# Optimization experiments

Measured on AMD Instinct MI355X. Metric: run time of the kernel, lower is better.

The kernel has to match this reference:

```python
import jax, jax.numpy as jnp
import numpy as np
import functools

N, D, R, E, L, C, MAXDEG = 40000, 128, 3, 640000, 2, 40, 512
BN_EPS = 1e-5


def setup_inputs():
    ks = iter(jax.random.split(jax.random.key(0), 40))
    nrm = lambda s, sc=0.05: jax.random.normal(next(ks), s, dtype=jnp.float32) * sc
    x = jax.random.normal(next(ks), (N, D), dtype=jnp.float32)
    edge_indices = jax.random.randint(next(ks), (R, 2, E), 0, N, dtype=jnp.int32)
    out_emb = nrm((L, MAXDEG, D)).at[:, 0].set(0.0)  # padding_idx=0 -> zero row
    in_emb = nrm((L, MAXDEG, D)).at[:, 0].set(0.0)
    return dict(
        x=x, edge_indices=edge_indices,
        W_src=nrm((L, D, D)), b_src=nrm((L, D)),
        W_dst=nrm((L, D, D)), b_dst=nrm((L, D)),
        W_outf=nrm((L, D)), b_outf=nrm((L,)),
        W_inf=nrm((L, D)), b_inf=nrm((L,)),
        W_fc=nrm((L, D, D)), b_fc=nrm((L, D)),
        bn_gamma=jnp.ones((L, D), jnp.float32), bn_beta=jnp.zeros((L, D), jnp.float32),
        out_deg_emb=out_emb, in_deg_emb=in_emb,
        out_mask=jnp.ones((R, N), jnp.float32), out_mask_bias=jnp.zeros((R, N), jnp.float32),
        in_mask=jnp.ones((R, N), jnp.float32), in_mask_bias=jnp.zeros((R, N), jnp.float32),
        alpha=jnp.float32(0.5), tau=jnp.float32(0.0),
        W_lin=nrm((D, C)), b_lin=nrm((C,)),
    )


def _forward(x, W_src, b_src, W_dst, b_dst, W_outf, b_outf, W_inf, b_inf,
             W_fc, b_fc, bn_gamma, bn_beta, out_deg_emb, in_deg_emb,
             out_mask, out_mask_bias, in_mask, in_mask_bias, alpha, tau,
             W_lin, b_lin, edge_indices):
    seg = lambda d, i: jax.ops.segment_sum(d, i, num_segments=N)
    # source builds I with arange(0, N-1): identity with last diagonal entry missing
    i_mask = (jnp.arange(N) < N - 1).astype(jnp.float32)[:, None]

    rel = []
    for r in range(R):
        row, col = edge_indices[r, 0], edge_indices[r, 1]
        ones = jnp.ones(E, jnp.float32)
        out_deg, in_deg = seg(ones, row), seg(ones, col)
        ods = jnp.where(out_deg > 0, 1.0 / jnp.sqrt(jnp.maximum(out_deg, 1.0)), 0.0)
        ids_ = jnp.where(in_deg > 0, 1.0 / jnp.sqrt(jnp.maximum(in_deg, 1.0)), 0.0)
        # 'dir' norm: D_out^{-1/2} A D_in^{-1/2}; the transposed adj shares the same edge weights
        w = ods[row] * ids_[col]
        rel.append((row, col, w,
                    jnp.clip(out_deg, 0, MAXDEG - 1).astype(jnp.int32),
                    jnp.clip(in_deg, 0, MAXDEG - 1).astype(jnp.int32)))

    def spmm(r_, y):  # adj_norm @ y : gather cols, scatter-add to rows
        row, col, w = rel[r_][0], rel[r_][1], rel[r_][2]
        return seg(w[:, None] * y[col], row)

    def spmm_t(r_, y):  # adj_norm^T @ y
        row, col, w = rel[r_][0], rel[r_][1], rel[r_][2]
        return seg(w[:, None] * y[row], col)

    def dirichlet(mm, y):
        x1 = y / (jnp.sum(jnp.abs(y), axis=1, keepdims=True) + 1e-12)  # row_l1_normalize
        x1sq = x1 * x1
        return (i_mask * x1sq + mm(x1sq)) - 2.0 * ((i_mask * x1 + mm(x1)) * x1 - x1sq)

    eff_tau = jnp.exp(tau) + 0.1

    def conv(l, h):
        out = jnp.zeros((N, D), h.dtype)
        cis, cos_ = [], []
        for r in range(R):
            mm = functools.partial(spmm, r)
            mmt = functools.partial(spmm_t, r)
            out_nei, in_nei = mm(h), mmt(h)
            e_out, e_in = dirichlet(mm, h), dirichlet(mmt, h)
            c_out = (-e_out + out_deg_emb[l][rel[r][3]]) @ W_outf[l] + b_outf[l]  # [N]
            c_in = (-e_in + in_deg_emb[l][rel[r][4]]) @ W_inf[l] + b_inf[l]
            cm = jax.nn.softmax(jnp.stack([c_out, c_in], axis=1) / eff_tau, axis=1)  # tau_softmax
            c_out = cm[:, 0] * out_mask[r] + out_mask_bias[r]
            c_in = cm[:, 1] * in_mask[r] + in_mask_bias[r]
            out = out + c_out[:, None] * (out_nei @ W_src[l] + b_src[l]) \
                      + c_in[:, None] * (in_nei @ W_dst[l] + b_dst[l])
            cis.append(c_in)
            cos_.append(c_out)
        out = out / R
        # F.pad(x,(0,dim-x.shape[1])) is a no-op since input_dim == output_dim
        output = out + alpha * (h @ W_fc[l] + b_fc[l])
        mu, var = jnp.mean(output, axis=0), jnp.var(output, axis=0)  # BatchNorm1d (train mode)
        output = (output - mu) / jnp.sqrt(var + BN_EPS) * bn_gamma[l] + bn_beta[l]
        return output, jnp.mean(jnp.stack(cis), 0)[:, None], jnp.mean(jnp.stack(cos_), 0)[:, None]

    pos_h, neg_h = x, x
    pos_hs, neg_hs, gs, cins, couts = [], [], [], [], []
    for l in range(L):
        ph, ci, co = conv(l, pos_h)
        ph = jax.nn.relu(ph)  # jumping_knowledge truthy -> relu every layer; dropout p=0
        perm = jax.random.permutation(jax.random.key(100 + l), N)  # torch.randperm
        nh, _, _ = conv(l, neg_h[perm])
        nh = jax.nn.relu(nh)
        pos_h, neg_h = ph, nh
        pos_hs.append(ph)
        neg_hs.append(nh)
        gs.append(jnp.mean(ph, axis=0, keepdims=True))
        cins.append(ci)
        couts.append(co)
    c_ins = jnp.mean(jnp.stack(cins), 0)
    c_outs = jnp.mean(jnp.stack(couts), 0)
    jk = functools.reduce(jnp.maximum, pos_hs)  # JumpingKnowledge mode='max'
    logp = jax.nn.log_softmax(jk @ W_lin + b_lin, axis=1)
    return (logp, c_ins, c_outs, *pos_hs, *neg_hs, *gs)


def reference(x, edge_indices, W_src, b_src, W_dst, b_dst, W_outf, b_outf,
              W_inf, b_inf, W_fc, b_fc, bn_gamma, bn_beta, out_deg_emb,
              in_deg_emb, out_mask, out_mask_bias, in_mask, in_mask_bias,
              alpha, tau, W_lin, b_lin):
    return _forward(x, W_src, b_src, W_dst, b_dst, W_outf, b_outf, W_inf, b_inf,
                    W_fc, b_fc, bn_gamma, bn_beta, out_deg_emb, in_deg_emb,
                    out_mask, out_mask_bias, in_mask, in_mask_bias, alpha, tau,
                    W_lin, b_lin, edge_indices)
```

## Files before the change

### kernel.cpp

```cpp
#include <hip/hip_runtime.h>

constexpr int Nn = 40000;
constexpr int Dd = 128;
constexpr int Rr = 3;
constexpr int Ee = 640000;
constexpr int Ll = 2;
constexpr int Cc = 40;
constexpr int MAXD = 512;
constexpr float BN_EPS = 1e-5f;

constexpr int RB_ELEMS = 1024;
constexpr int RB_NB = (Nn + RB_ELEMS - 1) / RB_ELEMS;
constexpr int RB_BINS = 256;

constexpr int EB_ELEMS = 4096;
constexpr int EB_NB = (Ee + EB_ELEMS - 1) / EB_ELEMS;
constexpr int EB_H = 256 * EB_NB;

constexpr int HR_BINS = 13334;
constexpr int HR_PAD = 13344;
constexpr int HR_SB = 16;
constexpr int HR_CHUNK = (Ee + HR_SB - 1) / HR_SB;

__device__ __forceinline__ unsigned rotl32(unsigned x, int d) { return (x << d) | (x >> (32 - d)); }

__device__ void threefry2x32(unsigned k0, unsigned k1, unsigned c0, unsigned c1,
                             unsigned& o0, unsigned& o1) {
  unsigned ks2 = k0 ^ k1 ^ 0x1BD11BDAu;
  unsigned x0 = c0 + k0, x1 = c1 + k1;
#define TFR4(a,b,c,d2) \
  x0 += x1; x1 = rotl32(x1,a);  x1 ^= x0; \
  x0 += x1; x1 = rotl32(x1,b);  x1 ^= x0; \
  x0 += x1; x1 = rotl32(x1,c);  x1 ^= x0; \
  x0 += x1; x1 = rotl32(x1,d2); x1 ^= x0;
  TFR4(13,15,26,6);  x0 += k1;  x1 += ks2 + 1u;
  TFR4(17,29,16,24); x0 += ks2; x1 += k0 + 2u;
  TFR4(13,15,26,6);  x0 += k0;  x1 += k1 + 3u;
  TFR4(17,29,16,24); x0 += k1;  x1 += ks2 + 4u;
  TFR4(13,15,26,6);  x0 += ks2; x1 += k0 + 5u;
#undef TFR4
  o0 = x0; o1 = x1;
}

__global__ void k_genkeys(unsigned* __restrict__ keys, unsigned seed, int rounds,
                          int* __restrict__ vout, int doIota) {
  int i = blockIdx.x * blockDim.x + threadIdx.x;
  if (i >= Nn) return;
  unsigned k0 = 0u, k1 = seed, sk0 = 0u, sk1 = 0u;
  for (int rd = 0; rd < rounds; rd++) {
    unsigned a0, a1, b0, b1;
    threefry2x32(k0, k1, 0u, 0u, a0, a1);
    threefry2x32(k0, k1, 0u, 1u, b0, b1);
    sk0 = b0; sk1 = b1;
    k0 = a0; k1 = a1;
  }
  unsigned o0, o1;
  threefry2x32(sk0, sk1, 0u, (unsigned)i, o0, o1);
  keys[i] = o0 ^ o1;
  if (doIota) vout[i] = i;
}

__global__ void k_rhist(const unsigned* __restrict__ keys, int* __restrict__ hist, int shift) {
  __shared__ int lh[RB_BINS];
  int t = threadIdx.x;
  lh[t] = 0;
  __syncthreads();
  int base = blockIdx.x * RB_ELEMS;
  for (int i = t; i < RB_ELEMS; i += 256) {
    int g = base + i;
    if (g < Nn) atomicAdd(&lh[(keys[g] >> shift) & 255], 1);
  }
  __syncthreads();
  hist[t * RB_NB + blockIdx.x] = lh[t];
}

__device__ void scan_body(const int* cnt, int* off, int n, int items) {
  int t = threadIdx.x;
  int lo = t * items, hi = min(lo + items, n);
  int s = 0;
  for (int i = lo; i < hi; i++) s += cnt[i];
  int lane = t & 63, wid = t >> 6;
  int sc = s;
#pragma unroll
  for (int o = 1; o < 64; o <<= 1) {
    int v = __shfl_up(sc, o);
    if (lane >= o) sc += v;
  }
  __shared__ int wsum[16], woff[16];
  if (lane == 63) wsum[wid] = sc;
  __syncthreads();
  if (t == 0) {
    int a = 0;
    for (int w = 0; w < 16; w++) { woff[w] = a; a += wsum[w]; }
    off[n] = a;
  }
  __syncthreads();
  int run = woff[wid] + sc - s;
  for (int i = lo; i < hi; i++) {
    int v = cnt[i];
    off[i] = run;
    run += v;
  }
}

__global__ __launch_bounds__(1024) void k_scanN(const int* __restrict__ cnt, int* __restrict__ off,
                                                int n, int items) {
  scan_body(cnt, off, n, items);
}

__global__ __launch_bounds__(1024) void k_scan6(const int* __restrict__ odeg, const int* __restrict__ ideg,
                                                int* __restrict__ csr_off, int* __restrict__ csc_off) {
  int b = blockIdx.x;
  const int* cnt = (b < 3) ? (odeg + b * Nn) : (ideg + (b - 3) * Nn);
  int* off = (b < 3) ? (csr_off + b * (Nn + 1)) : (csc_off + (b - 3) * (Nn + 1));
  scan_body(cnt, off, Nn, (Nn + 1023) / 1024);
}

__global__ void k_rscatter(const unsigned* __restrict__ keys, const int* __restrict__ vals,
                           const int* __restrict__ scanned, int shift,
                           unsigned* __restrict__ okeys, int* __restrict__ ovals) {
  __shared__ int running[RB_BINS];
  __shared__ int wcount[4][RB_BINS];
  __shared__ int dbase[RB_BINS];
  int t = threadIdx.x;
  int lane = t & 63, w = t >> 6;
  running[t] = 0;
  dbase[t] = scanned[t * RB_NB + blockIdx.x];
  int base = blockIdx.x * RB_ELEMS;
  for (int rnd = 0; rnd < 4; rnd++) {
#pragma unroll
    for (int q = 0; q < 4; q++) wcount[q][t] = 0;
    __syncthreads();
    int g = base + rnd * 256 + t;
    bool valid = g < Nn;
    unsigned key = valid ? keys[g] : 0u;
    int d = (key >> shift) & 255;
    unsigned long long bb = __ballot(valid);
    unsigned long long mask = bb;
#pragma unroll
    for (int k = 0; k < 8; k++) {
      bool b = (d >> k) & 1;
      unsigned long long tt = __ballot(b && valid);
      mask &= b ? tt : ~tt;
    }
    mask &= bb;
    int riw = __popcll(mask & ((1ull << lane) - 1ull));
    int cnt_ = __popcll(mask);
    if (valid && riw == 0) wcount[w][d] = cnt_;
    __syncthreads();
    if (valid) {
      int prior = 0;
#pragma unroll
      for (int ww = 0; ww < 4; ww++) if (ww < w) prior += wcount[ww][d];
      int gp = dbase[d] + running[d] + prior + riw;
      okeys[gp] = key;
      ovals[gp] = vals[g];
    }
    __syncthreads();
    running[t] += wcount[0][t] + wcount[1][t] + wcount[2][t] + wcount[3][t];
    __syncthreads();
  }
}

__global__ void k_permrows(const float* __restrict__ src, const int* __restrict__ perm,
                           float* __restrict__ dst) {
  int row = blockIdx.x * 8 + (threadIdx.x >> 5);
  int lane = threadIdx.x & 31;
  if (row >= Nn) return;
  int p = perm[row];
  ((float4*)(dst + (size_t)row * Dd))[lane] = ((const float4*)(src + (size_t)p * Dd))[lane];
}

__global__ __launch_bounds__(256) void k_hist2(const int* __restrict__ ei, int* __restrict__ partials) {
  __shared__ int lh[HR_BINS];
  int bid = blockIdx.x;
  int sb = bid % HR_SB;
  int range = (bid / HR_SB) % 3;
  int j = bid / (3 * HR_SB);
  int rel = j >> 1, which = j & 1;
  const int* src = ei + (size_t)rel * 2 * Ee + (size_t)which * Ee;
  int lo = range * HR_BINS;
  for (int i = threadIdx.x; i < HR_BINS; i += 256) lh[i] = 0;
  __syncthreads();
  int e0 = sb * HR_CHUNK, e1 = min(e0 + HR_CHUNK, Ee);
  for (int e = e0 + threadIdx.x; e < e1; e += 256) {
    int v = src[e] - lo;
    if (v >= 0 && v < HR_BINS) atomicAdd(&lh[v], 1);
  }
  __syncthreads();
  int* dst = partials + (size_t)bid * HR_PAD;
  for (int i = threadIdx.x; i < HR_BINS; i += 256) dst[i] = lh[i];
}

__global__ void k_hreduce(const int* __restrict__ partials, int* __restrict__ odeg,
                          int* __restrict__ ideg) {
  int idx = blockIdx.x * 256 + threadIdx.x;
  if (idx >= 6 * Nn) return;
  int j = idx / Nn, bin = idx - j * Nn;
  int range = bin / HR_BINS, off = bin - range * HR_BINS;
  const int* p = partials + (size_t)((j * 3 + range) * HR_SB) * HR_PAD + off;
  int sum = 0;
#pragma unroll
  for (int b = 0; b < HR_SB; b++) sum += p[(size_t)b * HR_PAD];
  int rel = j >> 1;
  (j & 1 ? ideg : odeg)[rel * Nn + bin] = sum;
}

__global__ void k_degnorm(const int* __restrict__ odeg, const int* __restrict__ ideg,
                          float* __restrict__ ods, float* __restrict__ ids,
                          int* __restrict__ odix, int* __restrict__ idix) {
  int idx = blockIdx.x * blockDim.x + threadIdx.x;
  if (idx >= Rr * Nn) return;
  int od = odeg[idx], id_ = ideg[idx];
  ods[idx] = od > 0 ? 1.0f / sqrtf((float)od) : 0.0f;
  ids[idx] = id_ > 0 ? 1.0f / sqrtf((float)id_) : 0.0f;
  odix[idx] = od < MAXD - 1 ? od : MAXD - 1;
  idix[idx] = id_ < MAXD - 1 ? id_ : MAXD - 1;
}

__global__ void k_pack(const int* __restrict__ ei, unsigned* __restrict__ pcsr,
                       unsigned* __restrict__ pcsc) {
  int idx = blockIdx.x * 256 + threadIdx.x;
  if (idx >= 3 * Ee) return;
  int r = idx / Ee, e = idx - r * Ee;
  const int* base = ei + (size_t)r * 2 * Ee;
  unsigned rw = (unsigned)base[e], cl = (unsigned)base[Ee + e];
  pcsr[idx] = (rw << 16) | cl;
  pcsc[idx] = (cl << 16) | rw;
}

__global__ __launch_bounds__(256) void k_ehist(const unsigned* __restrict__ pin,
                                               int* __restrict__ hist, int shift) {
  __shared__ int lh[256];
  int a = blockIdx.x / EB_NB, blk = blockIdx.x % EB_NB;
  const unsigned* src = pin + (size_t)a * Ee;
  lh[threadIdx.x] = 0;
  __syncthreads();
  int base = blk * EB_ELEMS;
  for (int i = threadIdx.x; i < EB_ELEMS; i += 256) {
    int g = base + i;
    if (g < Ee) atomicAdd(&lh[(src[g] >> shift) & 255], 1);
  }
  __syncthreads();
  hist[(size_t)a * EB_H + threadIdx.x * EB_NB + blk] = lh[threadIdx.x];
}

__global__ __launch_bounds__(1024) void k_escan6(const int* __restrict__ hist, int* __restrict__ esc) {
  int a = blockIdx.x;
  scan_body(hist + (size_t)a * EB_H, esc + (size_t)a * (EB_H + 1), EB_H, (EB_H + 1023) / 1024);
}

__global__ __launch_bounds__(256) void k_escatter(const unsigned* __restrict__ pin,
                                                  const int* __restrict__ esc, int shift,
                                                  unsigned* __restrict__ pout) {
  __shared__ int running[256];
  __shared__ int wcount[4][256];
  __shared__ int dbase[256];
  int a = blockIdx.x / EB_NB, blk = blockIdx.x % EB_NB;
  const unsigned* src = pin + (size_t)a * Ee;
  unsigned* dst = pout + (size_t)a * Ee;
  int t = threadIdx.x;
  int lane = t & 63, w = t >> 6;
  running[t] = 0;
  dbase[t] = esc[(size_t)a * (EB_H + 1) + t * EB_NB + blk];
  int base = blk * EB_ELEMS;
  for (int rnd = 0; rnd < 16; rnd++) {
#pragma unroll
    for (int q = 0; q < 4; q++) wcount[q][t] = 0;
    __syncthreads();
    int g = base + rnd * 256 + t;
    bool valid = g < Ee;
    unsigned key = valid ? src[g] : 0u;
    int d = (key >> shift) & 255;
    unsigned long long bb = __ballot(valid);
    unsigned long long mask = bb;
#pragma unroll
    for (int k = 0; k < 8; k++) {
      bool b = (d >> k) & 1;
      unsigned long long tt = __ballot(b && valid);
      mask &= b ? tt : ~tt;
    }
    mask &= bb;
    int riw = __popcll(mask & ((1ull << lane) - 1ull));
    int cnt_ = __popcll(mask);
    if (valid && riw == 0) wcount[w][d] = cnt_;
    __syncthreads();
    if (valid) {
      int prior = 0;
#pragma unroll
      for (int ww = 0; ww < 4; ww++) if (ww < w) prior += wcount[ww][d];
      int gp = dbase[d] + running[d] + prior + riw;
      dst[gp] = key;
    }
    __syncthreads();
    running[t] += wcount[0][t] + wcount[1][t] + wcount[2][t] + wcount[3][t];
    __syncthreads();
  }
}

__global__ void k_rowscalar(const float* __restrict__ h, const float* __restrict__ Wfo,
                            const float* __restrict__ Wfi, float4* __restrict__ aux) {
  int wid = (blockIdx.x * blockDim.x + threadIdx.x) >> 6;
  int lane = threadIdx.x & 63;
  if (wid >= Nn) return;
  float2 a = ((const float2*)(h + (size_t)wid * Dd))[lane];
  float2 wo = ((const float2*)Wfo)[lane];
  float2 wi = ((const float2*)Wfi)[lane];
  float l1 = fabsf(a.x) + fabsf(a.y);
  float so = a.x * a.x * wo.x + a.y * a.y * wo.y;
  float si = a.x * a.x * wi.x + a.y * a.y * wi.y;
#pragma unroll
  for (int o = 32; o; o >>= 1) {
    l1 += __shfl_xor(l1, o);
    so += __shfl_xor(so, o);
    si += __shfl_xor(si, o);
  }
  if (lane == 0) {
    float ri = 1.0f / (l1 + 1e-12f);
    aux[wid] = make_float4(ri, ri * ri * so, ri * ri * si, 0.f);
  }
}

__global__ void k_lut(const float* __restrict__ eo, const float* __restrict__ ei_,
                      const float* __restrict__ Wfo, const float* __restrict__ Wfi,
                      float* __restrict__ luto, float* __restrict__ luti) {
  int wid = (blockIdx.x * blockDim.x + threadIdx.x) >> 6;
  int lane = threadIdx.x & 63;
  if (wid >= MAXD) return;
  float2 a = ((const float2*)(eo + (size_t)wid * Dd))[lane];
  float2 b = ((const float2*)(ei_ + (size_t)wid * Dd))[lane];
  float2 wo = ((const float2*)Wfo)[lane];
  float2 wi = ((const float2*)Wfi)[lane];
  float so = a.x * wo.x + a.y * wo.y;
  float si = b.x * wi.x + b.y * wi.y;
#pragma unroll
  for (int o = 32; o; o >>= 1) { so += __shfl_xor(so, o); si += __shfl_xor(si, o); }
  if (lane == 0) { luto[wid] = so; luti[wid] = si; }
}

__global__ __launch_bounds__(512) void k_csrdir3(
    const int* __restrict__ csr_off, const unsigned* __restrict__ pcsr,
    const int* __restrict__ csc_off, const unsigned* __restrict__ pcsc,
    const float* __restrict__ ods_r, const float* __restrict__ ids_r,
    const float4* __restrict__ aux, const float* __restrict__ h,
    const float* __restrict__ Wfo, const float* __restrict__ Wfi,
    const float* __restrict__ luto, const float* __restrict__ luti,
    const int* __restrict__ odix, const int* __restrict__ idix,
    const float* __restrict__ bo, const float* __restrict__ bi,
    const float* __restrict__ taup,
    const float* __restrict__ omask, const float* __restrict__ omaskb,
    const float* __restrict__ imask, const float* __restrict__ imaskb,
    float* __restrict__ Tout, float* __restrict__ Tin,
    float* __restrict__ sco, float* __restrict__ sci,
    float* __restrict__ co_acc, float* __restrict__ ci_acc,
    int first, int is_pos) {
  __shared__ float lq[8], lp[8], lc[8];
  int t = threadIdx.x;
  int wv = t >> 6, lane = t & 63;
  int dir = wv >> 2;
  int n = blockIdx.x * 4 + (wv & 3);
  const int* off = dir ? csc_off : csr_off;
  const unsigned* nbrp = dir ? pcsc : pcsr;
  const float* scn = dir ? ods_r : ids_r;
  float a_self = (dir ? ids_r : ods_r)[n];
  const float* Wf = dir ? Wfi : Wfo;
  int s0 = off[n], s1 = off[n + 1];
  int hl = lane & 31, half = lane >> 5;
  float4 wf4 = ((const float4*)Wf)[hl];
  float4 hn4 = ((const float4*)(h + (size_t)n * Dd))[hl];
  float rn = aux[n].x;
  float4 s = make_float4(0.f, 0.f, 0.f, 0.f);
  float4 pa = make_float4(0.f, 0.f, 0.f, 0.f);
  float qacc = 0.f;
  for (int base = s0; base < s1; base += 64) {
    int eidx = base + lane;
    bool valid = eidx < s1;
    int mi = valid ? (int)(pcsr[0], nbrp[eidx] & 0xFFFFu) : 0;
    float4 av = valid ? aux[mi] : make_float4(0.f, 0.f, 0.f, 0.f);
    float scv = valid ? scn[mi] : 0.f;
    float qsel = dir ? av.z : av.y;
    int cnt = min(64, s1 - base);
    for (int j = half; j < cnt; j += 2) {
      int m = __shfl(mi, j);
      float sc = __shfl(scv, j);
      float rm = __shfl(av.x, j);
      float qv = __shfl(qsel, j);
      float w = a_self * sc;
      float wrm = w * rm;
      float4 hv = ((const float4*)(h + (size_t)m * Dd))[hl];
      s.x += w * hv.x; s.y += w * hv.y; s.z += w * hv.z; s.w += w * hv.w;
      pa.x += wrm * hv.x; pa.y += wrm * hv.y; pa.z += wrm * hv.z; pa.w += wrm * hv.w;
      qacc += w * qv;
    }
  }
  s.x += __shfl_xor(s.x, 32); s.y += __shfl_xor(s.y, 32);
  s.z += __shfl_xor(s.z, 32); s.w += __shfl_xor(s.w, 32);
  pa.x += __shfl_xor(pa.x, 32); pa.y += __shfl_xor(pa.y, 32);
  pa.z += __shfl_xor(pa.z, 32); pa.w += __shfl_xor(pa.w, 32);
  qacc += __shfl_xor(qacc, 32);
  float pd = rn * (hn4.x * wf4.x * pa.x + hn4.y * wf4.y * pa.y +
                   hn4.z * wf4.z * pa.z + hn4.w * wf4.w * pa.w);
#pragma unroll
  for (int o = 16; o; o >>= 1) pd += __shfl_xor(pd, o);
  if (lane == 0) { lq[wv] = qacc; lp[wv] = pd; }
  __syncthreads();
  if (t < 4) {
    int nn = blockIdx.x * 4 + t;
    float Qo_ = lq[t], Po_ = lp[t], Qi_ = lq[4 + t], Pi_ = lp[4 + t];
    float4 a2 = aux[nn];
    float im = (nn < Nn - 1) ? 1.0f : 0.0f;
    float so_ = luto[odix[nn]] + bo[0] - (Qo_ - 2.0f * Po_ + (2.0f - im) * a2.y);
    float si_ = luti[idix[nn]] + bi[0] - (Qi_ - 2.0f * Pi_ + (2.0f - im) * a2.z);
    float tt = expf(taup[0]) + 0.1f;
    float aa = so_ / tt, bb = si_ / tt;
    float mm = fmaxf(aa, bb);
    float ea = expf(aa - mm), eb = expf(bb - mm);
    float inv = 1.0f / (ea + eb);
    float co = ea * inv * omask[nn] + omaskb[nn];
    float ci = eb * inv * imask[nn] + imaskb[nn];
    lc[t] = co; lc[4 + t] = ci;
    if (first) { sco[nn] = co; sci[nn] = ci; }
    else       { sco[nn] += co; sci[nn] += ci; }
    if (is_pos) { co_acc[nn] += co; ci_acc[nn] += ci; }
  }
  __syncthreads();
  float c = lc[wv];
  if (lane < 32) {
    float* T = dir ? Tin : Tout;
    size_t o = (size_t)n * Dd;
    float4 v = make_float4(c * s.x, c * s.y, c * s.z, c * s.w);
    if (!first) {
      float4 old = ((const float4*)(T + o))[hl];
      v.x += old.x; v.y += old.y; v.z += old.z; v.w += old.w;
    }
    ((float4*)(T + o))[hl] = v;
  }
}

__global__ __launch_bounds__(256) void k_gemmconv(
    const float* __restrict__ Tout, const float* __restrict__ Tin, const float* __restrict__ h,
    const float* __restrict__ Wsrc, const float* __restrict__ Wdst, const float* __restrict__ Wfc,
    const float* __restrict__ bsrc, const float* __restrict__ bdst, const float* __restrict__ bfc,
    const float* __restrict__ sco, const float* __restrict__ sci,
    const float* __restrict__ alphap, float* __restrict__ pre) {
  __shared__ float Asm[64][36];
  __shared__ float Bsm[32][132];
  int t = threadIdx.x;
  int rg = t >> 5, cg = t & 31;
  int m0 = blockIdx.x * 64;
  int arow = t >> 2, aq = t & 3;
  float alpha = alphap[0];
  float acc[8][4];
#pragma unroll
  for (int r = 0; r < 8; r++)
#pragma unroll
    for (int c = 0; c < 4; c++) acc[r][c] = 0.f;
  for (int kt = 0; kt < 12; kt++) {
    int sec = kt >> 2, kc = (kt & 3) * 32;
    const float* Ap = sec == 0 ? Tout : (sec == 1 ? Tin : h);
    const float* Wp = sec == 0 ? Wsrc : (sec == 1 ? Wdst : Wfc);
    float sA = (sec == 2) ? alpha : (1.0f / (float)Rr);
    __syncthreads();
    {
      const float4* src = (const float4*)(Ap + (size_t)(m0 + arow) * Dd + kc + aq * 8);
      float4 v0 = src[0], v1 = src[1];
      float4* d0 = (float4*)&Asm[arow][aq * 8];
      d0[0] = make_float4(v0.x * sA, v0.y * sA, v0.z * sA, v0.w * sA);
      d0[1] = make_float4(v1.x * sA, v1.y * sA, v1.z * sA, v1.w * sA);
    }
#pragma unroll
    for (int j = 0; j < 4; j++) {
      int idx = t + j * 256;
      int k = idx >> 5, d4 = idx & 31;
      *(float4*)&Bsm[k][d4 * 4] = *(const float4*)(Wp + (size_t)(kc + k) * Dd + d4 * 4);
    }
    __syncthreads();
#pragma unroll
    for (int kk = 0; kk < 32; kk += 4) {
      float4 af[8], bf[4];
#pragma unroll
      for (int r = 0; r < 8; r++) af[r] = *(const float4*)&Asm[rg * 8 + r][kk];
#pragma unroll
      for (int j = 0; j < 4; j++) bf[j] = *(const float4*)&Bsm[kk + j][cg * 4];
#pragma unroll
      for (int r = 0; r < 8; r++) {
        const float* ap = (const float*)&af[r];
#pragma unroll
        for (int j = 0; j < 4; j++) {
          const float* bp = (const float*)&bf[j];
          acc[r][0] += ap[j] * bp[0];
          acc[r][1] += ap[j] * bp[1];
          acc[r][2] += ap[j] * bp[2];
          acc[r][3] += ap[j] * bp[3];
        }
      }
    }
  }
  float4 vb1 = *(const float4*)(bsrc + cg * 4);
  float4 vb2 = *(const float4*)(bdst + cg * 4);
  float4 vbf = *(const float4*)(bfc + cg * 4);
#pragma unroll
  for (int r = 0; r < 8; r++) {
    int row = m0 + rg * 8 + r;
    size_t o = (size_t)row * Dd + cg * 4;
    float s1 = sco[row] * (1.0f / (float)Rr), s2 = sci[row] * (1.0f / (float)Rr);
    float4 v;
    v.x = acc[r][0] + s1 * vb1.x + s2 * vb2.x + alpha * vbf.x;
    v.y = acc[r][1] + s1 * vb1.y + s2 * vb2.y + alpha * vbf.y;
    v.z = acc[r][2] + s1 * vb1.z + s2 * vb2.z + alpha * vbf.z;
    v.w = acc[r][3] + s1 * vb1.w + s2 * vb2.w + alpha * vbf.w;
    *(float4*)(pre + o) = v;
  }
}

__global__ void k_bnstats(const float* __restrict__ pre, float* __restrict__ sums) {
  __shared__ float ls[256], ls2[256];
  int c = threadIdx.x & 127, sub = threadIdx.x >> 7;
  float s = 0.f, s2 = 0.f;
  for (int n = blockIdx.x * 2 + sub; n < Nn; n += gridDim.x * 2) {
    float v = pre[(size_t)n * Dd + c];
    s += v; s2 += v * v;
  }
  ls[threadIdx.x] = s; ls2[threadIdx.x] = s2;
  __syncthreads();
  if (sub == 0) {
    atomicAdd(&sums[c], ls[c] + ls[c + 128]);
    atomicAdd(&sums[c + 128], ls2[c] + ls2[c + 128]);
  }
}

__global__ void k_bnapply(const float* __restrict__ pre, const float* __restrict__ sums,
                          const float* __restrict__ gamma, const float* __restrict__ beta,
                          float* __restrict__ hout, float* __restrict__ gs, int do_gs) {
  __shared__ float ls[256];
  int c = threadIdx.x & 127, sub = threadIdx.x >> 7;
  float mu = sums[c] * (1.0f / (float)Nn);
  float var = sums[c + 128] * (1.0f / (float)Nn) - mu * mu;
  float sc = gamma[c] / sqrtf(var + BN_EPS);
  float bt = beta[c];
  float g = 0.f;
  for (int n = blockIdx.x * 2 + sub; n < Nn; n += gridDim.x * 2) {
    float v = (pre[(size_t)n * Dd + c] - mu) * sc + bt;
    v = fmaxf(v, 0.f);
    hout[(size_t)n * Dd + c] = v;
    g += v;
  }
  if (do_gs) {
    ls[threadIdx.x] = g;
    __syncthreads();
    if (sub == 0) atomicAdd(&gs[c], (ls[c] + ls[c + 128]) * (1.0f / (float)Nn));
  }
}

__global__ void k_cio(const float* __restrict__ ci_acc, const float* __restrict__ co_acc,
                      float* __restrict__ cins, float* __restrict__ couts) {
  int n = blockIdx.x * blockDim.x + threadIdx.x;
  if (n < Nn) {
    cins[n] = ci_acc[n] * (1.0f / (float)(Ll * Rr));
    couts[n] = co_acc[n] * (1.0f / (float)(Ll * Rr));
  }
}

__global__ __launch_bounds__(64) void k_logp(const float* __restrict__ ph0, const float* __restrict__ ph1,
                      const float* __restrict__ Wlin, const float* __restrict__ blin,
                      float* __restrict__ logp) {
  __shared__ float jk[Dd];
  __shared__ float lg[Cc];
  int n = blockIdx.x, t = threadIdx.x;
  for (int d = t; d < Dd; d += 64) jk[d] = fmaxf(ph0[(size_t)n * Dd + d], ph1[(size_t)n * Dd + d]);
  __syncthreads();
  if (t < Cc) {
    float acc = blin[t];
    for (int k = 0; k < Dd; k++) acc += jk[k] * Wlin[k * Cc + t];
    lg[t] = acc;
  }
  __syncthreads();
  float m = -1e30f;
  for (int c = 0; c < Cc; c++) m = fmaxf(m, lg[c]);
  float s = 0.f;
  for (int c = 0; c < Cc; c++) s += expf(lg[c] - m);
  float lse = m + logf(s);
  if (t < Cc) logp[(size_t)n * Cc + t] = lg[t] - lse;
}

extern "C" void kernel_launch(void* const* d_in, const int* in_sizes, int n_in,
                              void* d_out, int out_size, void* d_ws, size_t ws_size,
                              hipStream_t stream) {
  const float* x      = (const float*)d_in[0];
  const int*   ei     = (const int*)d_in[1];
  const float* W_src  = (const float*)d_in[2];
  const float* b_src  = (const float*)d_in[3];
  const float* W_dst  = (const float*)d_in[4];
  const float* b_dst  = (const float*)d_in[5];
  const float* W_outf = (const float*)d_in[6];
  const float* b_outf = (const float*)d_in[7];
  const float* W_inf  = (const float*)d_in[8];
  const float* b_inf  = (const float*)d_in[9];
  const float* W_fc   = (const float*)d_in[10];
  const float* b_fc   = (const float*)d_in[11];
  const float* gamma  = (const float*)d_in[12];
  const float* beta   = (const float*)d_in[13];
  const float* oemb   = (const float*)d_in[14];
  const float* iemb   = (const float*)d_in[15];
  const float* omask  = (const float*)d_in[16];
  const float* omaskb = (const float*)d_in[17];
  const float* imask  = (const float*)d_in[18];
  const float* imaskb = (const float*)d_in[19];
  const float* alphap = (const float*)d_in[20];
  const float* taup   = (const float*)d_in[21];
  const float* Wlin   = (const float*)d_in[22];
  const float* blin   = (const float*)d_in[23];

  float* out   = (float*)d_out;
  float* logp  = out;
  float* cins  = logp + (size_t)Nn * Cc;
  float* couts = cins + Nn;
  float* ph0   = couts + Nn;
  float* ph1   = ph0 + (size_t)Nn * Dd;
  float* nh0   = ph1 + (size_t)Nn * Dd;
  float* nh1   = nh0 + (size_t)Nn * Dd;
  float* gs0   = nh1 + (size_t)Nn * Dd;
  float* gs1   = gs0 + Dd;

  char* p = (char*)d_ws;
  auto alloc = [&](size_t bytes) -> void* {
    void* q = (void*)p;
    p += (bytes + 255) & ~(size_t)255;
    return q;
  };
  float* pre   = (float*)alloc((size_t)Nn * Dd * 4);
  float* Tout  = (float*)alloc((size_t)Nn * Dd * 4);
  float* Tin   = (float*)alloc((size_t)Nn * Dd * 4);
  float* hperm = (float*)alloc((size_t)Nn * Dd * 4);
  unsigned* pbuf = (unsigned*)alloc((size_t)6 * Ee * 4);
  size_t qwords = (size_t)6 * Ee;
  size_t pwords = (size_t)(6 * 3 * HR_SB) * HR_PAD;
  unsigned* qbuf = (unsigned*)alloc((qwords > pwords ? qwords : pwords) * 4);
  int* partials = (int*)qbuf;
  int* csr_off = (int*)alloc((size_t)Rr * (Nn + 1) * 4);
  int* csc_off = (int*)alloc((size_t)Rr * (Nn + 1) * 4);
  int* odeg    = (int*)alloc((size_t)Rr * Nn * 4);
  int* ideg    = (int*)alloc((size_t)Rr * Nn * 4);
  float* ods   = (float*)alloc((size_t)Rr * Nn * 4);
  float* ids   = (float*)alloc((size_t)Rr * Nn * 4);
  int* odix    = (int*)alloc((size_t)Rr * Nn * 4);
  int* idix    = (int*)alloc((size_t)Rr * Nn * 4);
  float4* aux  = (float4*)alloc((size_t)Nn * 16);
  float* sco   = (float*)alloc((size_t)Nn * 4 * 2);
  float* sci   = sco + Nn;
  float* coacc = (float*)alloc((size_t)Nn * 4 * 2);
  float* ciacc = coacc + Nn;
  float* luto  = (float*)alloc(MAXD * 4);
  float* luti  = (float*)alloc(MAXD * 4);
  float* bnsum = (float*)alloc(256 * 4);
  unsigned* kbuf0 = (unsigned*)alloc((size_t)Nn * 4);
  unsigned* kbuf1 = (unsigned*)alloc((size_t)Nn * 4);
  int* vbuf0 = (int*)alloc((size_t)Nn * 4);
  int* vbuf1 = (int*)alloc((size_t)Nn * 4);
  int* rhist = (int*)alloc((size_t)(RB_BINS * RB_NB + 1) * 4);
  int* rscan = (int*)alloc((size_t)(RB_BINS * RB_NB + 1) * 4);
  int* ehist = (int*)alloc((size_t)6 * EB_H * 4);
  int* escan = (int*)alloc((size_t)6 * (EB_H + 1) * 4);

  k_hist2<<<6 * 3 * HR_SB, 256, 0, stream>>>(ei, partials);
  k_hreduce<<<(6 * Nn + 255) / 256, 256, 0, stream>>>(partials, odeg, ideg);
  k_degnorm<<<(Rr * Nn + 255) / 256, 256, 0, stream>>>(odeg, ideg, ods, ids, odix, idix);
  k_scan6<<<6, 1024, 0, stream>>>(odeg, ideg, csr_off, csc_off);
  k_pack<<<(3 * Ee + 255) / 256, 256, 0, stream>>>(ei, pbuf, pbuf + (size_t)3 * Ee);
  k_ehist<<<6 * EB_NB, 256, 0, stream>>>(pbuf, ehist, 16);
  k_escan6<<<6, 1024, 0, stream>>>(ehist, escan);
  k_escatter<<<6 * EB_NB, 256, 0, stream>>>(pbuf, escan, 16, qbuf);
  k_ehist<<<6 * EB_NB, 256, 0, stream>>>(qbuf, ehist, 24);
  k_escan6<<<6, 1024, 0, stream>>>(ehist, escan);
  k_escatter<<<6 * EB_NB, 256, 0, stream>>>(qbuf, escan, 24, pbuf);
  hipMemsetAsync(coacc, 0, (size_t)Nn * 4 * 2, stream);

  auto radix4 = [&]() {
    for (int pass = 0; pass < 4; pass++) {
      const unsigned* ik = (pass & 1) ? kbuf1 : kbuf0;
      const int*      iv = (pass & 1) ? vbuf1 : vbuf0;
      unsigned*       ok = (pass & 1) ? kbuf0 : kbuf1;
      int*            ov = (pass & 1) ? vbuf0 : vbuf1;
      int shift = pass * 8;
      k_rhist<<<RB_NB, 256, 0, stream>>>(ik, rhist, shift);
      k_scanN<<<1, 1024, 0, stream>>>(rhist, rscan, RB_BINS * RB_NB, (RB_BINS * RB_NB + 1023) / 1024);
      k_rscatter<<<RB_NB, 256, 0, stream>>>(ik, iv, rscan, shift, ok, ov);
    }
  };

  auto make_perm = [&](unsigned seed) {
    k_genkeys<<<(Nn + 255) / 256, 256, 0, stream>>>(kbuf0, seed, 1, vbuf0, 1);
    radix4();
    k_genkeys<<<(Nn + 255) / 256, 256, 0, stream>>>(kbuf0, seed, 2, vbuf0, 0);
    radix4();
  };

  auto conv = [&](int l, const float* hin, float* hout, float* gs, int is_pos) {
    const float* Wfo = W_outf + l * Dd;
    const float* Wfi = W_inf + l * Dd;
    k_rowscalar<<<Nn / 4, 256, 0, stream>>>(hin, Wfo, Wfi, aux);
    for (int r = 0; r < Rr; r++) {
      k_csrdir3<<<Nn / 4, 512, 0, stream>>>(csr_off + r * (Nn + 1), pbuf + (size_t)r * Ee,
                                            csc_off + r * (Nn + 1), pbuf + (size_t)(3 + r) * Ee,
                                            ods + r * Nn, ids + r * Nn, aux, hin, Wfo, Wfi,
                                            luto, luti, odix + r * Nn, idix + r * Nn,
                                            b_outf + l, b_inf + l, taup,
                                            omask + (size_t)r * Nn, omaskb + (size_t)r * Nn,
                                            imask + (size_t)r * Nn, imaskb + (size_t)r * Nn,
                                            Tout, Tin, sco, sci, coacc, ciacc,
                                            r == 0 ? 1 : 0, is_pos);
    }
    k_gemmconv<<<Nn / 64, 256, 0, stream>>>(Tout, Tin, hin,
                                            W_src + (size_t)l * Dd * Dd, W_dst + (size_t)l * Dd * Dd,
                                            W_fc + (size_t)l * Dd * Dd,
                                            b_src + l * Dd, b_dst + l * Dd, b_fc + l * Dd,
                                            sco, sci, alphap, pre);
    hipMemsetAsync(bnsum, 0, 256 * 4, stream);
    k_bnstats<<<256, 256, 0, stream>>>(pre, bnsum);
    if (is_pos) hipMemsetAsync(gs, 0, Dd * 4, stream);
    k_bnapply<<<256, 256, 0, stream>>>(pre, bnsum, gamma + l * Dd, beta + l * Dd, hout, gs, is_pos);
  };

  k_lut<<<MAXD / 4, 256, 0, stream>>>(oemb, iemb, W_outf, W_inf, luto, luti);
  conv(0, x, ph0, gs0, 1);
  make_perm(100u);
  k_permrows<<<Nn / 8, 256, 0, stream>>>(x, vbuf0, hperm);
  conv(0, hperm, nh0, nullptr, 0);

  k_lut<<<MAXD / 4, 256, 0, stream>>>(oemb + (size_t)MAXD * Dd, iemb + (size_t)MAXD * Dd,
                                      W_outf + Dd, W_inf + Dd, luto, luti);
  conv(1, ph0, ph1, gs1, 1);
  make_perm(101u);
  k_permrows<<<Nn / 8, 256, 0, stream>>>(nh0, vbuf0, hperm);
  conv(1, hperm, nh1, nullptr, 0);

  k_cio<<<(Nn + 255) / 256, 256, 0, stream>>>(ciacc, coacc, cins, couts);
  k_logp<<<Nn, 64, 0, stream>>>(ph0, ph1, Wlin, blin, logp);
}
```

Measured before the change: 2.473 ms.

## Fuse per-relation SpMM launches into one kernel and fold BN stats into GEMM

```diff
diff --git a/kernel.cpp b/kernel.cpp
--- a/kernel.cpp
+++ b/kernel.cpp
@@ -338,102 +338,109 @@
   if (lane == 0) { luto[wid] = so; luti[wid] = si; }
 }
 
-__global__ __launch_bounds__(512) void k_csrdir3(
-    const int* __restrict__ csr_off, const unsigned* __restrict__ pcsr,
-    const int* __restrict__ csc_off, const unsigned* __restrict__ pcsc,
-    const float* __restrict__ ods_r, const float* __restrict__ ids_r,
+__global__ __launch_bounds__(512) void k_csrdir4(
+    const int* __restrict__ csr_off_all, const int* __restrict__ csc_off_all,
+    const unsigned* __restrict__ pbuf,
+    const float* __restrict__ ods_all, const float* __restrict__ ids_all,
     const float4* __restrict__ aux, const float* __restrict__ h,
     const float* __restrict__ Wfo, const float* __restrict__ Wfi,
     const float* __restrict__ luto, const float* __restrict__ luti,
-    const int* __restrict__ odix, const int* __restrict__ idix,
+    const int* __restrict__ odix_all, const int* __restrict__ idix_all,
     const float* __restrict__ bo, const float* __restrict__ bi,
     const float* __restrict__ taup,
-    const float* __restrict__ omask, const float* __restrict__ omaskb,
-    const float* __restrict__ imask, const float* __restrict__ imaskb,
+    const float* __restrict__ omask_all, const float* __restrict__ omaskb_all,
+    const float* __restrict__ imask_all, const float* __restrict__ imaskb_all,
     float* __restrict__ Tout, float* __restrict__ Tin,
     float* __restrict__ sco, float* __restrict__ sci,
-    float* __restrict__ co_acc, float* __restrict__ ci_acc,
-    int first, int is_pos) {
+    float* __restrict__ co_acc, float* __restrict__ ci_acc, int is_pos) {
   __shared__ float lq[8], lp[8], lc[8];
   int t = threadIdx.x;
   int wv = t >> 6, lane = t & 63;
   int dir = wv >> 2;
   int n = blockIdx.x * 4 + (wv & 3);
-  const int* off = dir ? csc_off : csr_off;
-  const unsigned* nbrp = dir ? pcsc : pcsr;
-  const float* scn = dir ? ods_r : ids_r;
-  float a_self = (dir ? ids_r : ods_r)[n];
+  int hl = lane & 31, half = lane >> 5;
   const float* Wf = dir ? Wfi : Wfo;
-  int s0 = off[n], s1 = off[n + 1];
-  int hl = lane & 31, half = lane >> 5;
   float4 wf4 = ((const float4*)Wf)[hl];
   float4 hn4 = ((const float4*)(h + (size_t)n * Dd))[hl];
   float rn = aux[n].x;
-  float4 s = make_float4(0.f, 0.f, 0.f, 0.f);
-  float4 pa = make_float4(0.f, 0.f, 0.f, 0.f);
-  float qacc = 0.f;
-  for (int base = s0; base < s1; base += 64) {
-    int eidx = base + lane;
-    bool valid = eidx < s1;
-    int mi = valid ? (int)(pcsr[0], nbrp[eidx] & 0xFFFFu) : 0;
-    float4 av = valid ? aux[mi] : make_float4(0.f, 0.f, 0.f, 0.f);
-    float scv = valid ? scn[mi] : 0.f;
-    float qsel = dir ? av.z : av.y;
-    int cnt = min(64, s1 - base);
-    for (int j = half; j < cnt; j += 2) {
-      int m = __shfl(mi, j);
-      float sc = __shfl(scv, j);
-      float rm = __shfl(av.x, j);
-      float qv = __shfl(qsel, j);
-      float w = a_self * sc;
-      float wrm = w * rm;
-      float4 hv = ((const float4*)(h + (size_t)m * Dd))[hl];
-      s.x += w * hv.x; s.y += w * hv.y; s.z += w * hv.z; s.w += w * hv.w;
-      pa.x += wrm * hv.x; pa.y += wrm * hv.y; pa.z += wrm * hv.z; pa.w += wrm * hv.w;
-      qacc += w * qv;
-    }
-  }
-  s.x += __shfl_xor(s.x, 32); s.y += __shfl_xor(s.y, 32);
-  s.z += __shfl_xor(s.z, 32); s.w += __shfl_xor(s.w, 32);
-  pa.x += __shfl_xor(pa.x, 32); pa.y += __shfl_xor(pa.y, 32);
-  pa.z += __shfl_xor(pa.z, 32); pa.w += __shfl_xor(pa.w, 32);
-  qacc += __shfl_xor(qacc, 32);
-  float pd = rn * (hn4.x * wf4.x * pa.x + hn4.y * wf4.y * pa.y +
-                   hn4.z * wf4.z * pa.z + hn4.w * wf4.w * pa.w);
-#pragma unroll
-  for (int o = 16; o; o >>= 1) pd += __shfl_xor(pd, o);
-  if (lane == 0) { lq[wv] = qacc; lp[wv] = pd; }
-  __syncthreads();
+  float4 Tacc = make_float4(0.f, 0.f, 0.f, 0.f);
+  float scosum = 0.f, scisum = 0.f;
+
+  for (int r = 0; r < Rr; r++) {
+    const int* off = (dir ? csc_off_all : csr_off_all) + r * (Nn + 1);
+    const unsigned* nbrp = pbuf + (size_t)(dir ? 3 + r : r) * Ee;
+    const float* ods_r = ods_all + r * Nn;
+    const float* ids_r = ids_all + r * Nn;
+    const float* scn = dir ? ods_r : ids_r;
+    float a_self = (dir ? ids_r : ods_r)[n];
+    int s0 = off[n], s1 = off[n + 1];
+    float4 s = make_float4(0.f, 0.f, 0.f, 0.f);
+    float4 pa = make_float4(0.f, 0.f, 0.f, 0.f);
+    float qacc = 0.f;
+    for (int base = s0; base < s1; base += 64) {
+      int eidx = base + lane;
+      bool valid = eidx < s1;
+      int mi = valid ? (int)(nbrp[eidx] & 0xFFFFu) : 0;
+      float4 av = valid ? aux[mi] : make_float4(0.f, 0.f, 0.f, 0.f);
+      float scv = valid ? scn[mi] : 0.f;
+      float qsel = dir ? av.z : av.y;
+      int cnt = min(64, s1 - base);
+#pragma unroll 4
+      for (int j = half; j < cnt; j += 2) {
+        int m = __shfl(mi, j);
+        float sc = __shfl(scv, j);
+        float rm = __shfl(av.x, j);
+        float qv = __shfl(qsel, j);
+        float w = a_self * sc;
+        float wrm = w * rm;
+        float4 hv = ((const float4*)(h + (size_t)m * Dd))[hl];
+        s.x += w * hv.x; s.y += w * hv.y; s.z += w * hv.z; s.w += w * hv.w;
+        pa.x += wrm * hv.x; pa.y += wrm * hv.y; pa.z += wrm * hv.z; pa.w += wrm * hv.w;
+        qacc += w * qv;
+      }
+    }
+    s.x += __shfl_xor(s.x, 32); s.y += __shfl_xor(s.y, 32);
+    s.z += __shfl_xor(s.z, 32); s.w += __shfl_xor(s.w, 32);
+    pa.x += __shfl_xor(pa.x, 32); pa.y += __shfl_xor(pa.y, 32);
+    pa.z += __shfl_xor(pa.z, 32); pa.w += __shfl_xor(pa.w, 32);
+    qacc += __shfl_xor(qacc, 32);
+    float pd = rn * (hn4.x * wf4.x * pa.x + hn4.y * wf4.y * pa.y +
+                     hn4.z * wf4.z * pa.z + hn4.w * wf4.w * pa.w);
+#pragma unroll
+    for (int o = 16; o; o >>= 1) pd += __shfl_xor(pd, o);
+    if (lane == 0) { lq[wv] = qacc; lp[wv] = pd; }
+    __syncthreads();
+    if (t < 4) {
+      int nn = blockIdx.x * 4 + t;
+      float Qo_ = lq[t], Po_ = lp[t], Qi_ = lq[4 + t], Pi_ = lp[4 + t];
+      float4 a2 = aux[nn];
+      float im = (nn < Nn - 1) ? 1.0f : 0.0f;
+      float so_ = luto[odix_all[r * Nn + nn]] + bo[0] - (Qo_ - 2.0f * Po_ + (2.0f - im) * a2.y);
+      float si_ = luti[idix_all[r * Nn + nn]] + bi[0] - (Qi_ - 2.0f * Pi_ + (2.0f - im) * a2.z);
+      float tt = expf(taup[0]) + 0.1f;
+      float aa = so_ / tt, bb = si_ / tt;
+      float mm = fmaxf(aa, bb);
+      float ea = expf(aa - mm), eb = expf(bb - mm);
+      float inv = 1.0f / (ea + eb);
+      float co = ea * inv * omask_all[r * Nn + nn] + omaskb_all[r * Nn + nn];
+      float ci = eb * inv * imask_all[r * Nn + nn] + imaskb_all[r * Nn + nn];
+      lc[t] = co; lc[4 + t] = ci;
+      scosum += co; scisum += ci;
+    }
+    __syncthreads();
+    float c = lc[wv];
+    float vx = c * s.x, vy = c * s.y, vz = c * s.z, vw = c * s.w;
+    Tacc.x += vx; Tacc.y += vy; Tacc.z += vz; Tacc.w += vw;
+  }
+
+  if (lane < 32) {
+    float* T = dir ? Tin : Tout;
+    ((float4*)(T + (size_t)n * Dd))[hl] = Tacc;
+  }
   if (t < 4) {
     int nn = blockIdx.x * 4 + t;
-    float Qo_ = lq[t], Po_ = lp[t], Qi_ = lq[4 + t], Pi_ = lp[4 + t];
-    float4 a2 = aux[nn];
-    float im = (nn < Nn - 1) ? 1.0f : 0.0f;
-    float so_ = luto[odix[nn]] + bo[0] - (Qo_ - 2.0f * Po_ + (2.0f - im) * a2.y);
-    float si_ = luti[idix[nn]] + bi[0] - (Qi_ - 2.0f * Pi_ + (2.0f - im) * a2.z);
-    float tt = expf(taup[0]) + 0.1f;
-    float aa = so_ / tt, bb = si_ / tt;
-    float mm = fmaxf(aa, bb);
-    float ea = expf(aa - mm), eb = expf(bb - mm);
-    float inv = 1.0f / (ea + eb);
-    float co = ea * inv * omask[nn] + omaskb[nn];
-    float ci = eb * inv * imask[nn] + imaskb[nn];
-    lc[t] = co; lc[4 + t] = ci;
-    if (first) { sco[nn] = co; sci[nn] = ci; }
-    else       { sco[nn] += co; sci[nn] += ci; }
-    if (is_pos) { co_acc[nn] += co; ci_acc[nn] += ci; }
-  }
-  __syncthreads();
-  float c = lc[wv];
-  if (lane < 32) {
-    float* T = dir ? Tin : Tout;
-    size_t o = (size_t)n * Dd;
-    float4 v = make_float4(c * s.x, c * s.y, c * s.z, c * s.w);
-    if (!first) {
-      float4 old = ((const float4*)(T + o))[hl];
-      v.x += old.x; v.y += old.y; v.z += old.z; v.w += old.w;
-    }
-    ((float4*)(T + o))[hl] = v;
+    sco[nn] = scosum; sci[nn] = scisum;
+    if (is_pos) { co_acc[nn] += scosum; ci_acc[nn] += scisum; }
   }
 }
 
@@ -442,9 +449,10 @@
     const float* __restrict__ Wsrc, const float* __restrict__ Wdst, const float* __restrict__ Wfc,
     const float* __restrict__ bsrc, const float* __restrict__ bdst, const float* __restrict__ bfc,
     const float* __restrict__ sco, const float* __restrict__ sci,
-    const float* __restrict__ alphap, float* __restrict__ pre) {
+    const float* __restrict__ alphap, float* __restrict__ pre, float* __restrict__ bnsum) {
   __shared__ float Asm[64][36];
   __shared__ float Bsm[32][132];
+  __shared__ float lsum[128], lsum2[128];
   int t = threadIdx.x;
   int rg = t >> 5, cg = t & 31;
   int m0 = blockIdx.x * 64;
@@ -499,6 +507,7 @@
   float4 vb1 = *(const float4*)(bsrc + cg * 4);
   float4 vb2 = *(const float4*)(bdst + cg * 4);
   float4 vbf = *(const float4*)(bfc + cg * 4);
+  float ps[4] = {0.f, 0.f, 0.f, 0.f}, ps2[4] = {0.f, 0.f, 0.f, 0.f};
 #pragma unroll
   for (int r = 0; r < 8; r++) {
     int row = m0 + rg * 8 + r;
@@ -510,23 +519,19 @@
     v.z = acc[r][2] + s1 * vb1.z + s2 * vb2.z + alpha * vbf.z;
     v.w = acc[r][3] + s1 * vb1.w + s2 * vb2.w + alpha * vbf.w;
     *(float4*)(pre + o) = v;
-  }
-}
-
-__global__ void k_bnstats(const float* __restrict__ pre, float* __restrict__ sums) {
-  __shared__ float ls[256], ls2[256];
-  int c = threadIdx.x & 127, sub = threadIdx.x >> 7;
-  float s = 0.f, s2 = 0.f;
-  for (int n = blockIdx.x * 2 + sub; n < Nn; n += gridDim.x * 2) {
-    float v = pre[(size_t)n * Dd + c];
-    s += v; s2 += v * v;
-  }
-  ls[threadIdx.x] = s; ls2[threadIdx.x] = s2;
-  __syncthreads();
-  if (sub == 0) {
-    atomicAdd(&sums[c], ls[c] + ls[c + 128]);
-    atomicAdd(&sums[c + 128], ls2[c] + ls2[c + 128]);
-  }
+    ps[0] += v.x; ps[1] += v.y; ps[2] += v.z; ps[3] += v.w;
+    ps2[0] += v.x * v.x; ps2[1] += v.y * v.y; ps2[2] += v.z * v.z; ps2[3] += v.w * v.w;
+  }
+  if (t < 128) { lsum[t] = 0.f; lsum2[t] = 0.f; }
+  __syncthreads();
+#pragma unroll
+  for (int j = 0; j < 4; j++) {
+    atomicAdd(&lsum[cg * 4 + j], ps[j]);
+    atomicAdd(&lsum2[cg * 4 + j], ps2[j]);
+  }
+  __syncthreads();
+  if (t < 128) atomicAdd(&bnsum[t], lsum[t]);
+  else if (t < 256) atomicAdd(&bnsum[t], lsum2[t - 128]);
 }
 
 __global__ void k_bnapply(const float* __restrict__ pre, const float* __restrict__ sums,
@@ -699,24 +704,17 @@
     const float* Wfo = W_outf + l * Dd;
     const float* Wfi = W_inf + l * Dd;
     k_rowscalar<<<Nn / 4, 256, 0, stream>>>(hin, Wfo, Wfi, aux);
-    for (int r = 0; r < Rr; r++) {
-      k_csrdir3<<<Nn / 4, 512, 0, stream>>>(csr_off + r * (Nn + 1), pbuf + (size_t)r * Ee,
-                                            csc_off + r * (Nn + 1), pbuf + (size_t)(3 + r) * Ee,
-                                            ods + r * Nn, ids + r * Nn, aux, hin, Wfo, Wfi,
-                                            luto, luti, odix + r * Nn, idix + r * Nn,
-                                            b_outf + l, b_inf + l, taup,
-                                            omask + (size_t)r * Nn, omaskb + (size_t)r * Nn,
-                                            imask + (size_t)r * Nn, imaskb + (size_t)r * Nn,
-                                            Tout, Tin, sco, sci, coacc, ciacc,
-                                            r == 0 ? 1 : 0, is_pos);
-    }
+    k_csrdir4<<<Nn / 4, 512, 0, stream>>>(csr_off, csc_off, pbuf, ods, ids, aux, hin,
+                                          Wfo, Wfi, luto, luti, odix, idix,
+                                          b_outf + l, b_inf + l, taup,
+                                          omask, omaskb, imask, imaskb,
+                                          Tout, Tin, sco, sci, coacc, ciacc, is_pos);
+    hipMemsetAsync(bnsum, 0, 256 * 4, stream);
     k_gemmconv<<<Nn / 64, 256, 0, stream>>>(Tout, Tin, hin,
                                             W_src + (size_t)l * Dd * Dd, W_dst + (size_t)l * Dd * Dd,
                                             W_fc + (size_t)l * Dd * Dd,
                                             b_src + l * Dd, b_dst + l * Dd, b_fc + l * Dd,
-                                            sco, sci, alphap, pre);
-    hipMemsetAsync(bnsum, 0, 256 * 4, stream);
-    k_bnstats<<<256, 256, 0, stream>>>(pre, bnsum);
+                                            sco, sci, alphap, pre, bnsum);
     if (is_pos) hipMemsetAsync(gs, 0, Dd * 4, stream);
     k_bnapply<<<256, 256, 0, stream>>>(pre, bnsum, gamma + l * Dd, beta + l * Dd, hout, gs, is_pos);
   };
```

Result: slower. 2.832 ms (+14.5%).
